# Performance work log

Measured on AMD Instinct MI355X. Metric: run time of the kernel, lower is better.

The kernel has to match this reference:

```python
import jax, jax.numpy as jnp
import numpy as np

N_NODES = 100000
N_EDGES = 1200000
N_GRAPHS = 1000
HID = 64
OUT = 4
ALPHA_FLAG = 0.03
NEG_SLOPE = 0.2


def _glorot(key, shape):
    fan_in, fan_out = shape[0], shape[-1]
    lim = (6.0 / (fan_in + fan_out)) ** 0.5
    return jax.random.uniform(key, shape, jnp.float32, -lim, lim)


def setup_inputs() -> dict:
    key = jax.random.key(0)
    ks = jax.random.split(key, 32)
    inp = {
        "x": jax.random.normal(ks[0], (N_NODES, 8), jnp.float32),
        "edge_index": jax.random.randint(ks[1], (2, N_EDGES), 0, N_NODES, jnp.int32),
        "batch": jnp.sort(jax.random.randint(ks[2], (N_NODES,), 0, N_GRAPHS, jnp.int32)),
        "climber": jax.random.normal(ks[3], (N_GRAPHS, 6), jnp.float32),
        # lin_in
        "W_in": _glorot(ks[4], (6, HID)), "b_in": jnp.zeros((HID,), jnp.float32),
        # climber_embed: LayerNorm(6) + Linear(6,64)
        "ln_g": jnp.ones((6,), jnp.float32), "ln_b": jnp.zeros((6,), jnp.float32),
        "W_c": _glorot(ks[5], (6, HID)), "b_c": jnp.zeros((HID,), jnp.float32),
        # film1 / film2: Linear(64,128)
        "Wf1": _glorot(ks[6], (HID, 2 * HID)), "bf1": jnp.zeros((2 * HID,), jnp.float32),
        "Wf2": _glorot(ks[7], (HID, 2 * HID)), "bf2": jnp.zeros((2 * HID,), jnp.float32),
        # GATConv 1 (heads=1): lin weight, att_src, att_dst, bias
        "Wg1": _glorot(ks[8], (HID, HID)), "as1": _glorot(ks[9], (HID, 1))[:, 0],
        "ad1": _glorot(ks[10], (HID, 1))[:, 0], "bg1": jnp.zeros((HID,), jnp.float32),
        # GATConv 2
        "Wg2": _glorot(ks[11], (HID, HID)), "as2": _glorot(ks[12], (HID, 1))[:, 0],
        "ad2": _glorot(ks[13], (HID, 1))[:, 0], "bg2": jnp.zeros((HID,), jnp.float32),
        # cls head
        "Wc1": _glorot(ks[14], (HID, HID)), "bc1": jnp.zeros((HID,), jnp.float32),
        "Wc2": _glorot(ks[15], (HID, OUT)), "bc2": jnp.zeros((OUT,), jnp.float32),
        # flag head
        "Wh1": _glorot(ks[16], (2, 8)), "bh1": jnp.zeros((8,), jnp.float32),
        "Wh2": _glorot(ks[17], (8, OUT)), "bh2": jnp.zeros((OUT,), jnp.float32),
    }
    return inp


def _gat(h, src, dst, W, a_src, a_dst, bias, n):
    # PyG GATConv, heads=1, concat=False, self-loops already appended.
    z = h @ W                                    # [N, H]
    e = jax.nn.leaky_relu((z @ a_src)[src] + (z @ a_dst)[dst], NEG_SLOPE)  # [E]
    m = jax.ops.segment_max(e, dst, num_segments=n)
    ex = jnp.exp(e - m[dst])
    s = jax.ops.segment_sum(ex, dst, num_segments=n)
    alpha = ex / (s[dst] + 1e-16)
    out = jax.ops.segment_sum(alpha[:, None] * z[src], dst, num_segments=n)
    return out + bias


def reference(x, edge_index, batch, climber, W_in, b_in, ln_g, ln_b, W_c, b_c,
              Wf1, bf1, Wf2, bf2, Wg1, as1, ad1, bg1, Wg2, as2, ad2, bg2,
              Wc1, bc1, Wc2, bc2, Wh1, bh1, Wh2, bh2):
    n = x.shape[0]
    # add self loops (PyG GATConv default)
    loop = jnp.arange(n, dtype=edge_index.dtype)
    src = jnp.concatenate([edge_index[0], loop])
    dst = jnp.concatenate([edge_index[1], loop])

    x_cont, flags = x[:, :6], x[:, 6:8]
    h = x_cont @ W_in + b_in

    # climber embed: LayerNorm + Linear + ReLU
    mu = jnp.mean(climber, -1, keepdims=True)
    var = jnp.var(climber, -1, keepdims=True)
    cn = (climber - mu) * jax.lax.rsqrt(var + 1e-5) * ln_g + ln_b
    c = jax.nn.relu(cn @ W_c + b_c)

    def film(h, Wf, bf):
        gb = c @ Wf + bf
        gamma, beta = jnp.split(gb, 2, axis=-1)
        return h * (1.0 + gamma[batch]) + beta[batch]

    h = film(h, Wf1, bf1)
    h = jax.nn.relu(_gat(h, src, dst, Wg1, as1, ad1, bg1, n))
    h = film(h, Wf2, bf2)
    h = jax.nn.relu(_gat(h, src, dst, Wg2, as2, ad2, bg2, n))

    # cls head (dropout inactive in eval)
    cls = jax.nn.relu(h @ Wc1 + bc1) @ Wc2 + bc2
    flag = jax.nn.relu(flags @ Wh1 + bh1) @ Wh2 + bh2
    return cls + ALPHA_FLAG * flag
```

## Files before the change

### kernel.cpp

```cpp
#include <hip/hip_runtime.h>
#include <math.h>

#define N_NODES 100000
#define N_EDGES 1200000
#define N_GRAPHS 1000
#define HID 64
#define NBUCK 256
#define NPB   391
#define BCAP  8192
#define EDGE_CHUNK 16384
#define S3_BLOCKS ((N_EDGES + EDGE_CHUNK - 1) / EDGE_CHUNK)
#define LOG2E 1.4426950408889634f
#define N_TILES (N_NODES / 16)
#define MFMA_BLOCKS 391

typedef _Float16 half_t;
typedef __attribute__((ext_vector_type(4))) _Float16 half4;
typedef __attribute__((ext_vector_type(8))) _Float16 half8;
typedef __attribute__((ext_vector_type(4))) float floatx4;

__global__ void k_climber_film(const float* __restrict__ climber,
                               const float* __restrict__ ln_g, const float* __restrict__ ln_b,
                               const float* __restrict__ W_c, const float* __restrict__ b_c,
                               const float* __restrict__ Wf1, const float* __restrict__ bf1,
                               const float* __restrict__ Wf2, const float* __restrict__ bf2,
                               float* __restrict__ gb1, float* __restrict__ gb2,
                               int* __restrict__ bucket_fill) {
    __shared__ float cl[64];
    int g = blockIdx.x;
    int j = threadIdx.x;
    if (g == 0) {
        bucket_fill[j] = 0;
        bucket_fill[j + 128] = 0;
    }
    if (j < 64) {
        float v[6];
        float mu = 0.f;
        #pragma unroll
        for (int k = 0; k < 6; k++) { v[k] = climber[g*6+k]; mu += v[k]; }
        mu *= (1.f/6.f);
        float var = 0.f;
        #pragma unroll
        for (int k = 0; k < 6; k++) { float d = v[k]-mu; var += d*d; }
        var *= (1.f/6.f);
        float rs = rsqrtf(var + 1e-5f);
        float acc = b_c[j];
        #pragma unroll
        for (int k = 0; k < 6; k++) {
            float cn = (v[k]-mu)*rs*ln_g[k] + ln_b[k];
            acc += cn * W_c[k*64+j];
        }
        cl[j] = fmaxf(acc, 0.f);
    }
    __syncthreads();
    float a1 = bf1[j], a2 = bf2[j];
    #pragma unroll 8
    for (int k = 0; k < 64; k++) {
        float ck = cl[k];
        a1 += ck * Wf1[k*128+j];
        a2 += ck * Wf2[k*128+j];
    }
    gb1[g*128+j] = a1;
    gb2[g*128+j] = a2;
}


__global__ void k_bin(const int* __restrict__ ei, int* __restrict__ bucket_fill,
                      int* __restrict__ staged) {
    __shared__ int hist[NBUCK];
    __shared__ int cursor[NBUCK];
    for (int t = threadIdx.x; t < NBUCK; t += blockDim.x) hist[t] = 0;
    __syncthreads();
    int e0 = blockIdx.x * EDGE_CHUNK;
    int e1 = min(e0 + EDGE_CHUNK, N_EDGES);
    for (int e = e0 + threadIdx.x; e < e1; e += blockDim.x)
        atomicAdd(&hist[ei[N_EDGES + e] / NPB], 1);
    __syncthreads();
    if (threadIdx.x < NBUCK) {
        int hv = hist[threadIdx.x];
        int start = threadIdx.x * BCAP;
        if (hv) start += atomicAdd(&bucket_fill[threadIdx.x], hv);
        cursor[threadIdx.x] = start;
    }
    __syncthreads();
    for (int e = e0 + threadIdx.x; e < e1; e += blockDim.x) {
        int src = ei[e], dst = ei[N_EDGES + e];
        int b = dst / NPB;
        int ldst = dst - b * NPB;
        int pos = atomicAdd(&cursor[b], 1);
        staged[pos] = (ldst << 17) | src;
    }
}

__global__ void k_bcsr(const int* __restrict__ staged, const int* __restrict__ bucket_fill,
                       int* __restrict__ rowptr, int* __restrict__ csr_src) {
    __shared__ int bb[NBUCK];
    __shared__ int ldeg[NPB];
    __shared__ int sc[512];
    __shared__ int cursor[NPB];
    int b = blockIdx.x;
    if (threadIdx.x < NBUCK) bb[threadIdx.x] = bucket_fill[threadIdx.x];
    __syncthreads();
    for (int off = 1; off < NBUCK; off <<= 1) {
        int u = 0;
        if (threadIdx.x < NBUCK && threadIdx.x >= off) u = bb[threadIdx.x - off];
        __syncthreads();
        if (threadIdx.x < NBUCK) bb[threadIdx.x] += u;
        __syncthreads();
    }
    int bbase = (b == 0) ? 0 : bb[b-1];
    int bcnt  = bb[b] - bbase;
    const int* st = staged + b * BCAP;
    int n0 = b * NPB;
    int n1 = min(n0 + NPB, N_NODES);
    int nn = n1 - n0;
    for (int t = threadIdx.x; t < NPB; t += blockDim.x) ldeg[t] = 0;
    __syncthreads();
    for (int k = threadIdx.x; k < bcnt; k += blockDim.x)
        atomicAdd(&ldeg[st[k] >> 17], 1);
    __syncthreads();
    if (threadIdx.x < 512) sc[threadIdx.x] = (threadIdx.x < nn) ? ldeg[threadIdx.x] : 0;
    __syncthreads();
    for (int off = 1; off < 512; off <<= 1) {
        int u = 0;
        if (threadIdx.x < 512 && threadIdx.x >= off) u = sc[threadIdx.x - off];
        __syncthreads();
        if (threadIdx.x < 512) sc[threadIdx.x] += u;
        __syncthreads();
    }
    if (threadIdx.x < nn) {
        int pre = sc[threadIdx.x] - ldeg[threadIdx.x];
        rowptr[n0 + threadIdx.x] = bbase + pre;
        cursor[threadIdx.x] = bbase + pre;
    }
    if (b == 0 && threadIdx.x == 0) rowptr[N_NODES] = bb[NBUCK-1];
    __syncthreads();
    for (int k = threadIdx.x; k < bcnt; k += blockDim.x) {
        int v = st[k];
        int pos = atomicAdd(&cursor[v >> 17], 1);
        csr_src[pos] = v & 0x1FFFF;
    }
}

__global__ __launch_bounds__(256) void k_mfma_z1(
        const float* __restrict__ x, const int* __restrict__ batch,
        const float* __restrict__ W_in, const float* __restrict__ b_in,
        const float* __restrict__ gb1, const float* __restrict__ W,
        const float* __restrict__ a_src, const float* __restrict__ a_dst,
        half_t* __restrict__ z, float* __restrict__ es, float* __restrict__ ed) {
    __shared__ float Wi[384];
    __shared__ float bi[64];
    __shared__ half_t zl[4][16*64];
    for (int idx = threadIdx.x; idx < 384; idx += 256) Wi[idx] = W_in[idx];
    if (threadIdx.x < 64) bi[threadIdx.x] = b_in[threadIdx.x];
    int wave = threadIdx.x >> 6;
    int l    = threadIdx.x & 63;
    int c    = l & 15;
    int g    = l >> 4;
    half8 Bf[2][4];
    #pragma unroll
    for (int ko = 0; ko < 2; ko++) {
        #pragma unroll
        for (int nt = 0; nt < 4; nt++) {
            half8 bvec;
            #pragma unroll
            for (int j = 0; j < 8; j++)
                bvec[j] = (half_t)W[(ko*32 + g*8 + j)*64 + c + 16*nt];
            Bf[ko][nt] = bvec;
        }
    }
    float as4[4], ad4[4];
    #pragma unroll
    for (int nt = 0; nt < 4; nt++) {
        as4[nt] = a_src[c + 16*nt] * LOG2E;
        ad4[nt] = a_dst[c + 16*nt] * LOG2E;
    }
    __syncthreads();
    int nWaves = gridDim.x * 4;
    int wid = blockIdx.x * 4 + wave;
    half_t* zw = zl[wave];
    for (int t = wid; t < N_TILES; t += nWaves) {
        int m0 = t * 16;
        int i = m0 + c;
        float xv[6];
        #pragma unroll
        for (int kk = 0; kk < 6; kk++) xv[kk] = x[i*8 + kk];
        int bg_ = batch[i];
        half8 A[2];
        #pragma unroll
        for (int s = 0; s < 2; s++) {
            int bk = s*32 + g*8;
            float acc[8];
            #pragma unroll
            for (int j = 0; j < 8; j++) acc[j] = bi[bk + j];
            #pragma unroll
            for (int kk = 0; kk < 6; kk++) {
                float xk = xv[kk];
                float4 w0 = *(const float4*)&Wi[kk*64 + bk];
                float4 w1 = *(const float4*)&Wi[kk*64 + bk + 4];
                acc[0] += xk*w0.x; acc[1] += xk*w0.y;
                acc[2] += xk*w0.z; acc[3] += xk*w0.w;
                acc[4] += xk*w1.x; acc[5] += xk*w1.y;
                acc[6] += xk*w1.z; acc[7] += xk*w1.w;
            }
            const float4* gbv = (const float4*)(gb1 + bg_*128);
            float4 ga0 = gbv[bk/4],      ga1 = gbv[bk/4 + 1];
            float4 be0 = gbv[16 + bk/4], be1 = gbv[16 + bk/4 + 1];
            half8 hv;
            hv[0] = (half_t)(acc[0]*(1.f+ga0.x) + be0.x);
            hv[1] = (half_t)(acc[1]*(1.f+ga0.y) + be0.y);
            hv[2] = (half_t)(acc[2]*(1.f+ga0.z) + be0.z);
            hv[3] = (half_t)(acc[3]*(1.f+ga0.w) + be0.w);
            hv[4] = (half_t)(acc[4]*(1.f+ga1.x) + be1.x);
            hv[5] = (half_t)(acc[5]*(1.f+ga1.y) + be1.y);
            hv[6] = (half_t)(acc[6]*(1.f+ga1.z) + be1.z);
            hv[7] = (half_t)(acc[7]*(1.f+ga1.w) + be1.w);
            A[s] = hv;
        }
        floatx4 D[4];
        #pragma unroll
        for (int nt = 0; nt < 4; nt++) {
            floatx4 acc = {0.f, 0.f, 0.f, 0.f};
            acc = __builtin_amdgcn_mfma_f32_16x16x32_f16(A[0], Bf[0][nt], acc, 0, 0, 0);
            acc = __builtin_amdgcn_mfma_f32_16x16x32_f16(A[1], Bf[1][nt], acc, 0, 0, 0);
            D[nt] = acc;
        }
        #pragma unroll
        for (int r = 0; r < 4; r++) {
            float ps = D[0][r]*as4[0] + D[1][r]*as4[1] + D[2][r]*as4[2] + D[3][r]*as4[3];
            float pd = D[0][r]*ad4[0] + D[1][r]*ad4[1] + D[2][r]*ad4[2] + D[3][r]*ad4[3];
            #pragma unroll
            for (int off = 1; off < 16; off <<= 1) {
                ps += __shfl_xor(ps, off, 16);
                pd += __shfl_xor(pd, off, 16);
            }
            if (c == 0) {
                es[m0 + g*4 + r] = ps;
                ed[m0 + g*4 + r] = pd;
            }
        }
        #pragma unroll
        for (int nt = 0; nt < 4; nt++) {
            #pragma unroll
            for (int r = 0; r < 4; r++)
                zw[(g*4 + r)*64 + c + 16*nt] = (half_t)D[nt][r];
        }
        __asm__ __volatile__("s_waitcnt lgkmcnt(0)" ::: "memory");
        const half8* zr = (const half8*)zw;
        half8 v0 = zr[l*2];
        half8 v1 = zr[l*2 + 1];
        half8* zo = (half8*)(z + (size_t)m0 * 64);
        zo[l*2]     = v0;
        zo[l*2 + 1] = v1;
        __asm__ __volatile__("s_waitcnt lgkmcnt(0)" ::: "memory");
    }
}

__global__ __launch_bounds__(256) void k_mfma_z(
        const half_t* __restrict__ h, const float* __restrict__ W,
        const float* __restrict__ a_src, const float* __restrict__ a_dst,
        half_t* __restrict__ z, float* __restrict__ es, float* __restrict__ ed) {
    __shared__ half_t zl[4][16*64];
    int wave = threadIdx.x >> 6;
    int l    = threadIdx.x & 63;
    int c    = l & 15;
    int g    = l >> 4;
    half8 Bf[2][4];
    #pragma unroll
    for (int ko = 0; ko < 2; ko++) {
        #pragma unroll
        for (int nt = 0; nt < 4; nt++) {
            half8 b;
            #pragma unroll
            for (int j = 0; j < 8; j++)
                b[j] = (half_t)W[(ko*32 + g*8 + j)*64 + c + 16*nt];
            Bf[ko][nt] = b;
        }
    }
    float as4[4], ad4[4];
    #pragma unroll
    for (int nt = 0; nt < 4; nt++) {
        as4[nt] = a_src[c + 16*nt] * LOG2E;
        ad4[nt] = a_dst[c + 16*nt] * LOG2E;
    }
    int nWaves = gridDim.x * 4;
    int wid = blockIdx.x * 4 + wave;
    half_t* zw = zl[wave];
    for (int t = wid; t < N_TILES; t += nWaves) {
        int m0 = t * 16;
        const half8* hrow = (const half8*)(h + (size_t)(m0 + c) * 64);
        half8 A0 = hrow[g];
        half8 A1 = hrow[g + 4];
        floatx4 D[4];
        #pragma unroll
        for (int nt = 0; nt < 4; nt++) {
            floatx4 acc = {0.f, 0.f, 0.f, 0.f};
            acc = __builtin_amdgcn_mfma_f32_16x16x32_f16(A0, Bf[0][nt], acc, 0, 0, 0);
            acc = __builtin_amdgcn_mfma_f32_16x16x32_f16(A1, Bf[1][nt], acc, 0, 0, 0);
            D[nt] = acc;
        }
        #pragma unroll
        for (int r = 0; r < 4; r++) {
            float ps = D[0][r]*as4[0] + D[1][r]*as4[1] + D[2][r]*as4[2] + D[3][r]*as4[3];
            float pd = D[0][r]*ad4[0] + D[1][r]*ad4[1] + D[2][r]*ad4[2] + D[3][r]*ad4[3];
            #pragma unroll
            for (int off = 1; off < 16; off <<= 1) {
                ps += __shfl_xor(ps, off, 16);
                pd += __shfl_xor(pd, off, 16);
            }
            if (c == 0) {
                es[m0 + g*4 + r] = ps;
                ed[m0 + g*4 + r] = pd;
            }
        }
        #pragma unroll
        for (int nt = 0; nt < 4; nt++) {
            #pragma unroll
            for (int r = 0; r < 4; r++)
                zw[(g*4 + r)*64 + c + 16*nt] = (half_t)D[nt][r];
        }
        __asm__ __volatile__("s_waitcnt lgkmcnt(0)" ::: "memory");
        const half8* zr = (const half8*)zw;
        half8 v0 = zr[l*2];
        half8 v1 = zr[l*2 + 1];
        half8* zo = (half8*)(z + (size_t)m0 * 64);
        zo[l*2]     = v0;
        zo[l*2 + 1] = v1;
        __asm__ __volatile__("s_waitcnt lgkmcnt(0)" ::: "memory");
    }
}

__device__ __forceinline__ float4 h4_to_f4(half4 h) {
    float4 f;
    f.x = (float)h.x; f.y = (float)h.y; f.z = (float)h.z; f.w = (float)h.w;
    return f;
}

__global__ void k_agg(const int* __restrict__ rowptr, const int* __restrict__ csr_src,
                      const float* __restrict__ es, const float* __restrict__ ed,
                      const half_t* __restrict__ z, const float* __restrict__ bg,
                      const int* __restrict__ batch, const float* __restrict__ gb,
                      int apply_film, half_t* __restrict__ hout) {
    int tid = blockIdx.x * blockDim.x + threadIdx.x;
    int i  = tid >> 4;
    int sl = threadIdx.x & 15;
    if (i >= N_NODES) return;
    int beg = rowptr[i], end = rowptr[i+1];
    int deg = end - beg;
    float edi = ed[i];

    float e_self = es[i] + edi;
    e_self = fmaxf(e_self, 0.2f * e_self);

    int svA = 0, svB = 0;
    float exA = 0.f, exB = 0.f;
    if (sl < deg) {
        svA = csr_src[beg + sl];
        float v = es[svA] + edi;
        exA = exp2f(fmaxf(v, 0.2f * v));
    }
    if (16 + sl < deg) {
        svB = csr_src[beg + 16 + sl];
        float v = es[svB] + edi;
        exB = exp2f(fmaxf(v, 0.2f * v));
    }
    float s = exA + exB;
    #pragma unroll
    for (int off = 1; off < 16; off <<= 1)
        s += __shfl_xor(s, off, 16);
    float ex = exp2f(e_self);
    s += ex;

    const half4* z4 = (const half4*)z;
    float4 zi = h4_to_f4(z4[i*16 + sl]);
    float4 acc = {ex*zi.x, ex*zi.y, ex*zi.z, ex*zi.w};

    int lim = (deg < 32) ? deg : 32;
    int k = 0;
    for (; k + 8 <= lim; k += 8) {
        int a[8]; float e[8];
        if (k < 16) {
            #pragma unroll
            for (int j = 0; j < 8; j++) {
                a[j] = __shfl(svA, k+j, 16);
                e[j] = __shfl(exA, k+j, 16);
            }
        } else {
            #pragma unroll
            for (int j = 0; j < 8; j++) {
                a[j] = __shfl(svB, k-16+j, 16);
                e[j] = __shfl(exB, k-16+j, 16);
            }
        }
        half4 q[8];
        #pragma unroll
        for (int j = 0; j < 8; j++) q[j] = z4[a[j]*16 + sl];
        #pragma unroll
        for (int j = 0; j < 8; j++) {
            float4 r = h4_to_f4(q[j]);
            acc.x += e[j]*r.x; acc.y += e[j]*r.y;
            acc.z += e[j]*r.z; acc.w += e[j]*r.w;
        }
    }
    for (; k + 4 <= lim; k += 4) {
        int a[4]; float e[4];
        if (k < 16) {
            #pragma unroll
            for (int j = 0; j < 4; j++) {
                a[j] = __shfl(svA, k+j, 16);
                e[j] = __shfl(exA, k+j, 16);
            }
        } else {
            #pragma unroll
            for (int j = 0; j < 4; j++) {
                a[j] = __shfl(svB, k-16+j, 16);
                e[j] = __shfl(exB, k-16+j, 16);
            }
        }
        half4 q[4];
        #pragma unroll
        for (int j = 0; j < 4; j++) q[j] = z4[a[j]*16 + sl];
        #pragma unroll
        for (int j = 0; j < 4; j++) {
            float4 r = h4_to_f4(q[j]);
            acc.x += e[j]*r.x; acc.y += e[j]*r.y;
            acc.z += e[j]*r.z; acc.w += e[j]*r.w;
        }
    }
    for (; k < lim; k++) {
        int a; float e2;
        if (k < 16) { a = __shfl(svA, k, 16);    e2 = __shfl(exA, k, 16); }
        else        { a = __shfl(svB, k-16, 16); e2 = __shfl(exB, k-16, 16); }
        float4 zr = h4_to_f4(z4[a*16 + sl]);
        acc.x += e2*zr.x; acc.y += e2*zr.y; acc.z += e2*zr.z; acc.w += e2*zr.w;
    }
    for (int kk = beg + 32; kk < end; kk++) {
        int sv = csr_src[kk];
        float v = es[sv] + edi;
        float e2 = exp2f(fmaxf(v, 0.2f * v));
        s += e2;
        float4 zr = h4_to_f4(z4[sv*16 + sl]);
        acc.x += e2*zr.x; acc.y += e2*zr.y; acc.z += e2*zr.z; acc.w += e2*zr.w;
    }
    float inv = 1.f / (s + 1e-16f);
    float4 bg4 = ((const float4*)bg)[sl];
    float4 o;
    o.x = fmaxf(acc.x*inv + bg4.x, 0.f);
    o.y = fmaxf(acc.y*inv + bg4.y, 0.f);
    o.z = fmaxf(acc.z*inv + bg4.z, 0.f);
    o.w = fmaxf(acc.w*inv + bg4.w, 0.f);
    if (apply_film) {
        int g = batch[i];
        const float4* gb4 = (const float4*)gb;
        float4 ga = gb4[g*32 + sl];
        float4 be = gb4[g*32 + 16 + sl];
        o.x = o.x*(1.f+ga.x) + be.x;
        o.y = o.y*(1.f+ga.y) + be.y;
        o.z = o.z*(1.f+ga.z) + be.z;
        o.w = o.w*(1.f+ga.w) + be.w;
    }
    half4 hv;
    hv.x = (half_t)o.x; hv.y = (half_t)o.y; hv.z = (half_t)o.z; hv.w = (half_t)o.w;
    ((half4*)hout)[i*16 + sl] = hv;
}

__global__ __launch_bounds__(256) void k_head_mfma(
        const half_t* __restrict__ h, const float* __restrict__ x,
        const float* __restrict__ Wc1, const float* __restrict__ bc1,
        const float* __restrict__ Wc2, const float* __restrict__ bc2,
        const float* __restrict__ Wh1, const float* __restrict__ bh1,
        const float* __restrict__ Wh2, const float* __restrict__ bh2,
        float* __restrict__ out) {
    int l    = threadIdx.x & 63;
    int c    = l & 15;
    int g    = l >> 4;
    half8 Bf[2][4];
    #pragma unroll
    for (int ko = 0; ko < 2; ko++) {
        #pragma unroll
        for (int nt = 0; nt < 4; nt++) {
            half8 b;
            #pragma unroll
            for (int j = 0; j < 8; j++)
                b[j] = (half_t)Wc1[(ko*32 + g*8 + j)*64 + c + 16*nt];
            Bf[ko][nt] = b;
        }
    }
    float bc1v[4];
    float4 w2[4];
    #pragma unroll
    for (int nt = 0; nt < 4; nt++) {
        bc1v[nt] = bc1[c + 16*nt];
        w2[nt] = ((const float4*)Wc2)[c + 16*nt];
    }
    int nWaves = gridDim.x * 4;
    int wid = blockIdx.x * 4 + (threadIdx.x >> 6);
    for (int t = wid; t < N_TILES; t += nWaves) {
        int m0 = t * 16;
        const half8* hrow = (const half8*)(h + (size_t)(m0 + c) * 64);
        half8 A0 = hrow[g];
        half8 A1 = hrow[g + 4];
        floatx4 D[4];
        #pragma unroll
        for (int nt = 0; nt < 4; nt++) {
            floatx4 acc = {0.f, 0.f, 0.f, 0.f};
            acc = __builtin_amdgcn_mfma_f32_16x16x32_f16(A0, Bf[0][nt], acc, 0, 0, 0);
            acc = __builtin_amdgcn_mfma_f32_16x16x32_f16(A1, Bf[1][nt], acc, 0, 0, 0);
            D[nt] = acc;
        }
        #pragma unroll
        for (int r = 0; r < 4; r++) {
            float4 p = {0.f, 0.f, 0.f, 0.f};
            #pragma unroll
            for (int nt = 0; nt < 4; nt++) {
                float tv = fmaxf(D[nt][r] + bc1v[nt], 0.f);
                p.x += tv * w2[nt].x;
                p.y += tv * w2[nt].y;
                p.z += tv * w2[nt].z;
                p.w += tv * w2[nt].w;
            }
            #pragma unroll
            for (int off = 1; off < 16; off <<= 1) {
                p.x += __shfl_xor(p.x, off, 16);
                p.y += __shfl_xor(p.y, off, 16);
                p.z += __shfl_xor(p.z, off, 16);
                p.w += __shfl_xor(p.w, off, 16);
            }
            if (c == 0) {
                int m = m0 + g*4 + r;
                float f0 = x[m*8+6], f1 = x[m*8+7];
                float t8[8];
                #pragma unroll
                for (int q = 0; q < 8; q++)
                    t8[q] = fmaxf(f0*Wh1[q] + f1*Wh1[8+q] + bh1[q], 0.f);
                float fl[4];
                #pragma unroll
                for (int q = 0; q < 4; q++) {
                    float a = bh2[q];
                    #pragma unroll
                    for (int rr = 0; rr < 8; rr++) a += t8[rr]*Wh2[rr*4+q];
                    fl[q] = a;
                }
                float4 ov;
                ov.x = p.x + bc2[0] + 0.03f*fl[0];
                ov.y = p.y + bc2[1] + 0.03f*fl[1];
                ov.z = p.z + bc2[2] + 0.03f*fl[2];
                ov.w = p.w + bc2[3] + 0.03f*fl[3];
                ((float4*)out)[m] = ov;
            }
        }
    }
}

extern "C" void kernel_launch(void* const* d_in, const int* in_sizes, int n_in,
                              void* d_out, int out_size, void* d_ws, size_t ws_size,
                              hipStream_t stream) {
    const float* x       = (const float*)d_in[0];
    const int*   ei      = (const int*)  d_in[1];
    const int*   batch   = (const int*)  d_in[2];
    const float* climber = (const float*)d_in[3];
    const float* W_in    = (const float*)d_in[4];
    const float* b_in    = (const float*)d_in[5];
    const float* ln_g    = (const float*)d_in[6];
    const float* ln_b    = (const float*)d_in[7];
    const float* W_c     = (const float*)d_in[8];
    const float* b_c     = (const float*)d_in[9];
    const float* Wf1     = (const float*)d_in[10];
    const float* bf1     = (const float*)d_in[11];
    const float* Wf2     = (const float*)d_in[12];
    const float* bf2     = (const float*)d_in[13];
    const float* Wg1     = (const float*)d_in[14];
    const float* as1     = (const float*)d_in[15];
    const float* ad1     = (const float*)d_in[16];
    const float* bg1     = (const float*)d_in[17];
    const float* Wg2     = (const float*)d_in[18];
    const float* as2     = (const float*)d_in[19];
    const float* ad2     = (const float*)d_in[20];
    const float* bg2     = (const float*)d_in[21];
    const float* Wc1     = (const float*)d_in[22];
    const float* bc1     = (const float*)d_in[23];
    const float* Wc2     = (const float*)d_in[24];
    const float* bc2     = (const float*)d_in[25];
    const float* Wh1     = (const float*)d_in[26];
    const float* bh1     = (const float*)d_in[27];
    const float* Wh2     = (const float*)d_in[28];
    const float* bh2     = (const float*)d_in[29];
    float* out = (float*)d_out;
    float* ws  = (float*)d_ws;

    float*  gb1         = ws;
    float*  gb2         = gb1 + 128000;
    half_t* hbuf        = (half_t*)(gb2 + 128000);
    half_t* zbuf        = hbuf + 6400000;
    float*  es          = (float*)(zbuf + 6400000);
    float*  ed          = es + N_NODES;
    int*    rowptr      = (int*)(ed + N_NODES);
    int*    csr_src     = rowptr + N_NODES + 1;
    int*    bucket_fill = csr_src + N_EDGES;
    int*    staged      = bucket_fill + NBUCK;

    k_climber_film<<<N_GRAPHS, 128, 0, stream>>>(climber, ln_g, ln_b, W_c, b_c,
                                                 Wf1, bf1, Wf2, bf2, gb1, gb2,
                                                 bucket_fill);

    k_bin <<<S3_BLOCKS, 1024, 0, stream>>>(ei, bucket_fill, staged);
    k_bcsr<<<NBUCK, 1024, 0, stream>>>(staged, bucket_fill, rowptr, csr_src);

    int nodeBlocks = (N_NODES*16 + 255)/256;
    k_mfma_z1<<<MFMA_BLOCKS, 256, 0, stream>>>(x, batch, W_in, b_in, gb1, Wg1,
                                               as1, ad1, zbuf, es, ed);
    k_agg<<<nodeBlocks, 256, 0, stream>>>(rowptr, csr_src, es, ed, zbuf, bg1,
                                          batch, gb2, 1, hbuf);
    k_mfma_z<<<MFMA_BLOCKS, 256, 0, stream>>>(hbuf, Wg2, as2, ad2, zbuf, es, ed);
    k_agg<<<nodeBlocks, 256, 0, stream>>>(rowptr, csr_src, es, ed, zbuf, bg2,
                                          batch, gb2, 0, hbuf);
    k_head_mfma<<<MFMA_BLOCKS, 256, 0, stream>>>(hbuf, x, Wc1, bc1, Wc2, bc2,
                                                 Wh1, bh1, Wh2, bh2, out);
}
```

Baseline: 259.3 us.

## Fuse GAT projection and head into aggregation kernels, merge CSR build with layer-1 projection

Folds the second-layer linear projection and attention-logit computation into the first aggregation kernel, and the classification head into the second aggregation kernel, so the intermediate h buffer is never written to or reread from global memory. The CSR finalisation and the layer-1 projection now run as one launch, with different block ranges doing each. Weights are pre-swizzled to fp16 MFMA layout by two extra blocks in the climber kernel. Edge chunk size for binning is also reduced. This removes three kernel launches and some global round-trips, at the cost of extra __syncthreads in the aggregation blocks and double-buffered z/es/ed.

```diff
diff --git a/kernel.cpp b/kernel.cpp
--- a/kernel.cpp
+++ b/kernel.cpp
@@ -8,11 +8,12 @@
 #define NBUCK 256
 #define NPB   391
 #define BCAP  8192
-#define EDGE_CHUNK 16384
+#define EDGE_CHUNK 4096
 #define S3_BLOCKS ((N_EDGES + EDGE_CHUNK - 1) / EDGE_CHUNK)
+#define Z1_BLOCKS 98
 #define LOG2E 1.4426950408889634f
 #define N_TILES (N_NODES / 16)
-#define MFMA_BLOCKS 391
+#define AGG_BLOCKS (N_NODES / 16)
 
 typedef _Float16 half_t;
 typedef __attribute__((ext_vector_type(4))) _Float16 half4;
@@ -24,11 +25,27 @@
                                const float* __restrict__ W_c, const float* __restrict__ b_c,
                                const float* __restrict__ Wf1, const float* __restrict__ bf1,
                                const float* __restrict__ Wf2, const float* __restrict__ bf2,
+                               const float* __restrict__ Wg2, const float* __restrict__ Wc1,
                                float* __restrict__ gb1, float* __restrict__ gb2,
+                               half_t* __restrict__ Wp1, half_t* __restrict__ Wp2,
                                int* __restrict__ bucket_fill) {
     __shared__ float cl[64];
     int g = blockIdx.x;
     int j = threadIdx.x;
+    if (g >= N_GRAPHS) {
+        const float* Wsrc = (g == N_GRAPHS) ? Wg2 : Wc1;
+        half_t*      Wdst = (g == N_GRAPHS) ? Wp1 : Wp2;
+        for (int idx = j; idx < 4096; idx += 128) {
+            int jj = idx & 7;
+            int ko = (idx >> 3) & 1;
+            int l  = (idx >> 4) & 63;
+            int w  = idx >> 10;
+            int c  = l & 15;
+            int gg = l >> 4;
+            Wdst[idx] = (half_t)Wsrc[(ko*32 + gg*8 + jj)*64 + c + 16*w];
+        }
+        return;
+    }
     if (g == 0) {
         bucket_fill[j] = 0;
         bucket_fill[j + 128] = 0;
@@ -64,9 +81,9 @@
     gb2[g*128+j] = a2;
 }
 
-
-__global__ void k_bin(const int* __restrict__ ei, int* __restrict__ bucket_fill,
-                      int* __restrict__ staged) {
+__global__ __launch_bounds__(1024) void k_bin(const int* __restrict__ ei,
+                                              int* __restrict__ bucket_fill,
+                                              int* __restrict__ staged) {
     __shared__ int hist[NBUCK];
     __shared__ int cursor[NBUCK];
     for (int t = threadIdx.x; t < NBUCK; t += blockDim.x) hist[t] = 0;
@@ -92,66 +109,67 @@
     }
 }
 
-__global__ void k_bcsr(const int* __restrict__ staged, const int* __restrict__ bucket_fill,
-                       int* __restrict__ rowptr, int* __restrict__ csr_src) {
-    __shared__ int bb[NBUCK];
-    __shared__ int ldeg[NPB];
-    __shared__ int sc[512];
-    __shared__ int cursor[NPB];
-    int b = blockIdx.x;
-    if (threadIdx.x < NBUCK) bb[threadIdx.x] = bucket_fill[threadIdx.x];
-    __syncthreads();
-    for (int off = 1; off < NBUCK; off <<= 1) {
-        int u = 0;
-        if (threadIdx.x < NBUCK && threadIdx.x >= off) u = bb[threadIdx.x - off];
-        __syncthreads();
-        if (threadIdx.x < NBUCK) bb[threadIdx.x] += u;
-        __syncthreads();
-    }
-    int bbase = (b == 0) ? 0 : bb[b-1];
-    int bcnt  = bb[b] - bbase;
-    const int* st = staged + b * BCAP;
-    int n0 = b * NPB;
-    int n1 = min(n0 + NPB, N_NODES);
-    int nn = n1 - n0;
-    for (int t = threadIdx.x; t < NPB; t += blockDim.x) ldeg[t] = 0;
-    __syncthreads();
-    for (int k = threadIdx.x; k < bcnt; k += blockDim.x)
-        atomicAdd(&ldeg[st[k] >> 17], 1);
-    __syncthreads();
-    if (threadIdx.x < 512) sc[threadIdx.x] = (threadIdx.x < nn) ? ldeg[threadIdx.x] : 0;
-    __syncthreads();
-    for (int off = 1; off < 512; off <<= 1) {
-        int u = 0;
-        if (threadIdx.x < 512 && threadIdx.x >= off) u = sc[threadIdx.x - off];
-        __syncthreads();
-        if (threadIdx.x < 512) sc[threadIdx.x] += u;
-        __syncthreads();
-    }
-    if (threadIdx.x < nn) {
-        int pre = sc[threadIdx.x] - ldeg[threadIdx.x];
-        rowptr[n0 + threadIdx.x] = bbase + pre;
-        cursor[threadIdx.x] = bbase + pre;
-    }
-    if (b == 0 && threadIdx.x == 0) rowptr[N_NODES] = bb[NBUCK-1];
-    __syncthreads();
-    for (int k = threadIdx.x; k < bcnt; k += blockDim.x) {
-        int v = st[k];
-        int pos = atomicAdd(&cursor[v >> 17], 1);
-        csr_src[pos] = v & 0x1FFFF;
-    }
-}
-
-__global__ __launch_bounds__(256) void k_mfma_z1(
+__global__ __launch_bounds__(1024) void k_mid(
+        const int* __restrict__ staged, const int* __restrict__ bucket_fill,
+        int* __restrict__ rowptr, int* __restrict__ csr_src,
         const float* __restrict__ x, const int* __restrict__ batch,
         const float* __restrict__ W_in, const float* __restrict__ b_in,
         const float* __restrict__ gb1, const float* __restrict__ W,
         const float* __restrict__ a_src, const float* __restrict__ a_dst,
         half_t* __restrict__ z, float* __restrict__ es, float* __restrict__ ed) {
+    if (blockIdx.x < NBUCK) {
+        __shared__ int bb[NBUCK];
+        __shared__ int ldeg[NPB];
+        __shared__ int sc[512];
+        __shared__ int cursor[NPB];
+        int b = blockIdx.x;
+        if (threadIdx.x < NBUCK) bb[threadIdx.x] = bucket_fill[threadIdx.x];
+        __syncthreads();
+        for (int off = 1; off < NBUCK; off <<= 1) {
+            int u = 0;
+            if (threadIdx.x < NBUCK && threadIdx.x >= off) u = bb[threadIdx.x - off];
+            __syncthreads();
+            if (threadIdx.x < NBUCK) bb[threadIdx.x] += u;
+            __syncthreads();
+        }
+        int bbase = (b == 0) ? 0 : bb[b-1];
+        int bcnt  = bb[b] - bbase;
+        const int* st = staged + b * BCAP;
+        int n0 = b * NPB;
+        int n1 = min(n0 + NPB, N_NODES);
+        int nn = n1 - n0;
+        for (int t = threadIdx.x; t < NPB; t += blockDim.x) ldeg[t] = 0;
+        __syncthreads();
+        for (int k = threadIdx.x; k < bcnt; k += blockDim.x)
+            atomicAdd(&ldeg[st[k] >> 17], 1);
+        __syncthreads();
+        if (threadIdx.x < 512) sc[threadIdx.x] = (threadIdx.x < nn) ? ldeg[threadIdx.x] : 0;
+        __syncthreads();
+        for (int off = 1; off < 512; off <<= 1) {
+            int u = 0;
+            if (threadIdx.x < 512 && threadIdx.x >= off) u = sc[threadIdx.x - off];
+            __syncthreads();
+            if (threadIdx.x < 512) sc[threadIdx.x] += u;
+            __syncthreads();
+        }
+        if (threadIdx.x < nn) {
+            int pre = sc[threadIdx.x] - ldeg[threadIdx.x];
+            rowptr[n0 + threadIdx.x] = bbase + pre;
+            cursor[threadIdx.x] = bbase + pre;
+        }
+        if (b == 0 && threadIdx.x == 0) rowptr[N_NODES] = bb[NBUCK-1];
+        __syncthreads();
+        for (int k = threadIdx.x; k < bcnt; k += blockDim.x) {
+            int v = st[k];
+            int pos = atomicAdd(&cursor[v >> 17], 1);
+            csr_src[pos] = v & 0x1FFFF;
+        }
+        return;
+    }
     __shared__ float Wi[384];
     __shared__ float bi[64];
-    __shared__ half_t zl[4][16*64];
-    for (int idx = threadIdx.x; idx < 384; idx += 256) Wi[idx] = W_in[idx];
+    __shared__ __align__(16) half_t zl[16][1024];
+    for (int idx = threadIdx.x; idx < 384; idx += 1024) Wi[idx] = W_in[idx];
     if (threadIdx.x < 64) bi[threadIdx.x] = b_in[threadIdx.x];
     int wave = threadIdx.x >> 6;
     int l    = threadIdx.x & 63;
@@ -176,8 +194,8 @@
         ad4[nt] = a_dst[c + 16*nt] * LOG2E;
     }
     __syncthreads();
-    int nWaves = gridDim.x * 4;
-    int wid = blockIdx.x * 4 + wave;
+    int nWaves = Z1_BLOCKS * 16;
+    int wid = (blockIdx.x - NBUCK) * 16 + wave;
     half_t* zw = zl[wave];
     for (int t = wid; t < N_TILES; t += nWaves) {
         int m0 = t * 16;
@@ -256,99 +274,39 @@
     }
 }
 
-__global__ __launch_bounds__(256) void k_mfma_z(
-        const half_t* __restrict__ h, const float* __restrict__ W,
-        const float* __restrict__ a_src, const float* __restrict__ a_dst,
-        half_t* __restrict__ z, float* __restrict__ es, float* __restrict__ ed) {
-    __shared__ half_t zl[4][16*64];
-    int wave = threadIdx.x >> 6;
-    int l    = threadIdx.x & 63;
-    int c    = l & 15;
-    int g    = l >> 4;
-    half8 Bf[2][4];
-    #pragma unroll
-    for (int ko = 0; ko < 2; ko++) {
-        #pragma unroll
-        for (int nt = 0; nt < 4; nt++) {
-            half8 b;
-            #pragma unroll
-            for (int j = 0; j < 8; j++)
-                b[j] = (half_t)W[(ko*32 + g*8 + j)*64 + c + 16*nt];
-            Bf[ko][nt] = b;
-        }
-    }
-    float as4[4], ad4[4];
-    #pragma unroll
-    for (int nt = 0; nt < 4; nt++) {
-        as4[nt] = a_src[c + 16*nt] * LOG2E;
-        ad4[nt] = a_dst[c + 16*nt] * LOG2E;
-    }
-    int nWaves = gridDim.x * 4;
-    int wid = blockIdx.x * 4 + wave;
-    half_t* zw = zl[wave];
-    for (int t = wid; t < N_TILES; t += nWaves) {
-        int m0 = t * 16;
-        const half8* hrow = (const half8*)(h + (size_t)(m0 + c) * 64);
-        half8 A0 = hrow[g];
-        half8 A1 = hrow[g + 4];
-        floatx4 D[4];
-        #pragma unroll
-        for (int nt = 0; nt < 4; nt++) {
-            floatx4 acc = {0.f, 0.f, 0.f, 0.f};
-            acc = __builtin_amdgcn_mfma_f32_16x16x32_f16(A0, Bf[0][nt], acc, 0, 0, 0);
-            acc = __builtin_amdgcn_mfma_f32_16x16x32_f16(A1, Bf[1][nt], acc, 0, 0, 0);
-            D[nt] = acc;
-        }
-        #pragma unroll
-        for (int r = 0; r < 4; r++) {
-            float ps = D[0][r]*as4[0] + D[1][r]*as4[1] + D[2][r]*as4[2] + D[3][r]*as4[3];
-            float pd = D[0][r]*ad4[0] + D[1][r]*ad4[1] + D[2][r]*ad4[2] + D[3][r]*ad4[3];
-            #pragma unroll
-            for (int off = 1; off < 16; off <<= 1) {
-                ps += __shfl_xor(ps, off, 16);
-                pd += __shfl_xor(pd, off, 16);
-            }
-            if (c == 0) {
-                es[m0 + g*4 + r] = ps;
-                ed[m0 + g*4 + r] = pd;
-            }
-        }
-        #pragma unroll
-        for (int nt = 0; nt < 4; nt++) {
-            #pragma unroll
-            for (int r = 0; r < 4; r++)
-                zw[(g*4 + r)*64 + c + 16*nt] = (half_t)D[nt][r];
-        }
-        __asm__ __volatile__("s_waitcnt lgkmcnt(0)" ::: "memory");
-        const half8* zr = (const half8*)zw;
-        half8 v0 = zr[l*2];
-        half8 v1 = zr[l*2 + 1];
-        half8* zo = (half8*)(z + (size_t)m0 * 64);
-        zo[l*2]     = v0;
-        zo[l*2 + 1] = v1;
-        __asm__ __volatile__("s_waitcnt lgkmcnt(0)" ::: "memory");
-    }
-}
-
 __device__ __forceinline__ float4 h4_to_f4(half4 h) {
     float4 f;
     f.x = (float)h.x; f.y = (float)h.y; f.z = (float)h.z; f.w = (float)h.w;
     return f;
 }
 
-__global__ void k_agg(const int* __restrict__ rowptr, const int* __restrict__ csr_src,
-                      const float* __restrict__ es, const float* __restrict__ ed,
-                      const half_t* __restrict__ z, const float* __restrict__ bg,
-                      const int* __restrict__ batch, const float* __restrict__ gb,
-                      int apply_film, half_t* __restrict__ hout) {
-    int tid = blockIdx.x * blockDim.x + threadIdx.x;
-    int i  = tid >> 4;
-    int sl = threadIdx.x & 15;
-    if (i >= N_NODES) return;
+template<int MODE>
+__global__ __launch_bounds__(256) void k_agg_f(
+        const int* __restrict__ rowptr, const int* __restrict__ csr_src,
+        const float* __restrict__ es, const float* __restrict__ ed,
+        const half_t* __restrict__ z, const float* __restrict__ bg,
+        const int* __restrict__ batch, const float* __restrict__ gb,
+        const half_t* __restrict__ Wp,
+        const float* __restrict__ av_s, const float* __restrict__ av_d,
+        half_t* __restrict__ zout, float* __restrict__ es_o, float* __restrict__ ed_o,
+        const float* __restrict__ x,
+        const float* __restrict__ bc1, const float* __restrict__ Wc2,
+        const float* __restrict__ bc2,
+        const float* __restrict__ Wh1, const float* __restrict__ bh1,
+        const float* __restrict__ Wh2, const float* __restrict__ bh2,
+        float* __restrict__ out) {
+    __shared__ __align__(16) half_t h_l[1024];
+    __shared__ __align__(16) half_t zl16[1024];
+    __shared__ float red[4][16][4];
+    int tidb = threadIdx.x;
+    int il = tidb >> 4;
+    int sl = tidb & 15;
+    int m0 = blockIdx.x * 16;
+    int i = m0 + il;
+
     int beg = rowptr[i], end = rowptr[i+1];
     int deg = end - beg;
     float edi = ed[i];
-
     float e_self = es[i] + edi;
     e_self = fmaxf(e_self, 0.2f * e_self);
 
@@ -449,11 +407,11 @@
     o.y = fmaxf(acc.y*inv + bg4.y, 0.f);
     o.z = fmaxf(acc.z*inv + bg4.z, 0.f);
     o.w = fmaxf(acc.w*inv + bg4.w, 0.f);
-    if (apply_film) {
-        int g = batch[i];
+    if (MODE == 1) {
+        int gidx = batch[i];
         const float4* gb4 = (const float4*)gb;
-        float4 ga = gb4[g*32 + sl];
-        float4 be = gb4[g*32 + 16 + sl];
+        float4 ga = gb4[gidx*32 + sl];
+        float4 be = gb4[gidx*32 + 16 + sl];
         o.x = o.x*(1.f+ga.x) + be.x;
         o.y = o.y*(1.f+ga.y) + be.y;
         o.z = o.z*(1.f+ga.z) + be.z;
@@ -461,93 +419,97 @@
     }
     half4 hv;
     hv.x = (half_t)o.x; hv.y = (half_t)o.y; hv.z = (half_t)o.z; hv.w = (half_t)o.w;
-    ((half4*)hout)[i*16 + sl] = hv;
-}
-
-__global__ __launch_bounds__(256) void k_head_mfma(
-        const half_t* __restrict__ h, const float* __restrict__ x,
-        const float* __restrict__ Wc1, const float* __restrict__ bc1,
-        const float* __restrict__ Wc2, const float* __restrict__ bc2,
-        const float* __restrict__ Wh1, const float* __restrict__ bh1,
-        const float* __restrict__ Wh2, const float* __restrict__ bh2,
-        float* __restrict__ out) {
-    int l    = threadIdx.x & 63;
+    *(half4*)((char*)h_l + il*128 + ((sl*8) ^ ((il & 7) << 4))) = hv;
+
+    int l    = tidb & 63;
+    int wave = tidb >> 6;
     int c    = l & 15;
     int g    = l >> 4;
-    half8 Bf[2][4];
-    #pragma unroll
-    for (int ko = 0; ko < 2; ko++) {
-        #pragma unroll
-        for (int nt = 0; nt < 4; nt++) {
-            half8 b;
-            #pragma unroll
-            for (int j = 0; j < 8; j++)
-                b[j] = (half_t)Wc1[(ko*32 + g*8 + j)*64 + c + 16*nt];
-            Bf[ko][nt] = b;
-        }
-    }
-    float bc1v[4];
-    float4 w2[4];
-    #pragma unroll
-    for (int nt = 0; nt < 4; nt++) {
-        bc1v[nt] = bc1[c + 16*nt];
-        w2[nt] = ((const float4*)Wc2)[c + 16*nt];
-    }
-    int nWaves = gridDim.x * 4;
-    int wid = blockIdx.x * 4 + (threadIdx.x >> 6);
-    for (int t = wid; t < N_TILES; t += nWaves) {
-        int m0 = t * 16;
-        const half8* hrow = (const half8*)(h + (size_t)(m0 + c) * 64);
-        half8 A0 = hrow[g];
-        half8 A1 = hrow[g + 4];
-        floatx4 D[4];
-        #pragma unroll
-        for (int nt = 0; nt < 4; nt++) {
-            floatx4 acc = {0.f, 0.f, 0.f, 0.f};
-            acc = __builtin_amdgcn_mfma_f32_16x16x32_f16(A0, Bf[0][nt], acc, 0, 0, 0);
-            acc = __builtin_amdgcn_mfma_f32_16x16x32_f16(A1, Bf[1][nt], acc, 0, 0, 0);
-            D[nt] = acc;
-        }
+    const half8* wp = (const half8*)(Wp + ((size_t)tidb << 4));
+    half8 Bf0 = wp[0];
+    half8 Bf1 = wp[1];
+    float as_w = 0.f, ad_w = 0.f, bc1w = 0.f;
+    float4 w2w = {0.f, 0.f, 0.f, 0.f};
+    if (MODE == 1) {
+        as_w = av_s[c + 16*wave] * LOG2E;
+        ad_w = av_d[c + 16*wave] * LOG2E;
+    } else {
+        bc1w = bc1[c + 16*wave];
+        w2w  = ((const float4*)Wc2)[c + 16*wave];
+    }
+    __syncthreads();
+    half8 A0 = *(const half8*)((const char*)h_l + c*128 + ((g*16)      ^ ((c & 7) << 4)));
+    half8 A1 = *(const half8*)((const char*)h_l + c*128 + ((64 + g*16) ^ ((c & 7) << 4)));
+    floatx4 D = {0.f, 0.f, 0.f, 0.f};
+    D = __builtin_amdgcn_mfma_f32_16x16x32_f16(A0, Bf0, D, 0, 0, 0);
+    D = __builtin_amdgcn_mfma_f32_16x16x32_f16(A1, Bf1, D, 0, 0, 0);
+    if (MODE == 1) {
         #pragma unroll
         for (int r = 0; r < 4; r++) {
-            float4 p = {0.f, 0.f, 0.f, 0.f};
-            #pragma unroll
-            for (int nt = 0; nt < 4; nt++) {
-                float tv = fmaxf(D[nt][r] + bc1v[nt], 0.f);
-                p.x += tv * w2[nt].x;
-                p.y += tv * w2[nt].y;
-                p.z += tv * w2[nt].z;
-                p.w += tv * w2[nt].w;
-            }
+            float ps = D[r]*as_w, pd = D[r]*ad_w;
             #pragma unroll
             for (int off = 1; off < 16; off <<= 1) {
-                p.x += __shfl_xor(p.x, off, 16);
-                p.y += __shfl_xor(p.y, off, 16);
-                p.z += __shfl_xor(p.z, off, 16);
-                p.w += __shfl_xor(p.w, off, 16);
+                ps += __shfl_xor(ps, off, 16);
+                pd += __shfl_xor(pd, off, 16);
             }
             if (c == 0) {
-                int m = m0 + g*4 + r;
-                float f0 = x[m*8+6], f1 = x[m*8+7];
-                float t8[8];
+                red[wave][g*4 + r][0] = ps;
+                red[wave][g*4 + r][1] = pd;
+            }
+            zl16[(g*4 + r)*64 + c + 16*wave] = (half_t)D[r];
+        }
+        __syncthreads();
+        if (tidb < 16) {
+            es_o[m0 + tidb] = red[0][tidb][0] + red[1][tidb][0] + red[2][tidb][0] + red[3][tidb][0];
+            ed_o[m0 + tidb] = red[0][tidb][1] + red[1][tidb][1] + red[2][tidb][1] + red[3][tidb][1];
+        }
+        if (tidb < 128)
+            ((half8*)(zout + (size_t)m0 * 64))[tidb] = ((const half8*)zl16)[tidb];
+    } else {
+        #pragma unroll
+        for (int r = 0; r < 4; r++) {
+            float tv = fmaxf(D[r] + bc1w, 0.f);
+            float px = tv*w2w.x, py = tv*w2w.y, pz = tv*w2w.z, pw = tv*w2w.w;
+            #pragma unroll
+            for (int off = 1; off < 16; off <<= 1) {
+                px += __shfl_xor(px, off, 16);
+                py += __shfl_xor(py, off, 16);
+                pz += __shfl_xor(pz, off, 16);
+                pw += __shfl_xor(pw, off, 16);
+            }
+            if (c == 0) {
+                red[wave][g*4 + r][0] = px;
+                red[wave][g*4 + r][1] = py;
+                red[wave][g*4 + r][2] = pz;
+                red[wave][g*4 + r][3] = pw;
+            }
+        }
+        __syncthreads();
+        if (tidb < 16) {
+            int m = m0 + tidb;
+            float p0 = red[0][tidb][0] + red[1][tidb][0] + red[2][tidb][0] + red[3][tidb][0] + bc2[0];
+            float p1 = red[0][tidb][1] + red[1][tidb][1] + red[2][tidb][1] + red[3][tidb][1] + bc2[1];
+            float p2 = red[0][tidb][2] + red[1][tidb][2] + red[2][tidb][2] + red[3][tidb][2] + bc2[2];
+            float p3 = red[0][tidb][3] + red[1][tidb][3] + red[2][tidb][3] + red[3][tidb][3] + bc2[3];
+            float f0 = x[m*8+6], f1 = x[m*8+7];
+            float t8[8];
+            #pragma unroll
+            for (int q = 0; q < 8; q++)
+                t8[q] = fmaxf(f0*Wh1[q] + f1*Wh1[8+q] + bh1[q], 0.f);
+            float fl[4];
+            #pragma unroll
+            for (int q = 0; q < 4; q++) {
+                float a = bh2[q];
                 #pragma unroll
-                for (int q = 0; q < 8; q++)
-                    t8[q] = fmaxf(f0*Wh1[q] + f1*Wh1[8+q] + bh1[q], 0.f);
-                float fl[4];
-                #pragma unroll
-                for (int q = 0; q < 4; q++) {
-                    float a = bh2[q];
-                    #pragma unroll
-                    for (int rr = 0; rr < 8; rr++) a += t8[rr]*Wh2[rr*4+q];
-                    fl[q] = a;
-                }
-                float4 ov;
-                ov.x = p.x + bc2[0] + 0.03f*fl[0];
-                ov.y = p.y + bc2[1] + 0.03f*fl[1];
-                ov.z = p.z + bc2[2] + 0.03f*fl[2];
-                ov.w = p.w + bc2[3] + 0.03f*fl[3];
-                ((float4*)out)[m] = ov;
-            }
+                for (int rr = 0; rr < 8; rr++) a += t8[rr]*Wh2[rr*4+q];
+                fl[q] = a;
+            }
+            float4 ov;
+            ov.x = p0 + 0.03f*fl[0];
+            ov.y = p1 + 0.03f*fl[1];
+            ov.z = p2 + 0.03f*fl[2];
+            ov.w = p3 + 0.03f*fl[3];
+            ((float4*)out)[m] = ov;
         }
     }
 }
@@ -590,30 +552,39 @@
 
     float*  gb1         = ws;
     float*  gb2         = gb1 + 128000;
-    half_t* hbuf        = (half_t*)(gb2 + 128000);
-    half_t* zbuf        = hbuf + 6400000;
-    float*  es          = (float*)(zbuf + 6400000);
-    float*  ed          = es + N_NODES;
-    int*    rowptr      = (int*)(ed + N_NODES);
+    half_t* Wp1         = (half_t*)(gb2 + 128000);
+    half_t* Wp2         = Wp1 + 4096;
+    half_t* zA          = Wp2 + 4096;
+    half_t* zB          = zA + 6400000;
+    float*  es1         = (float*)(zB + 6400000);
+    float*  ed1         = es1 + N_NODES;
+    float*  es2         = ed1 + N_NODES;
+    float*  ed2         = es2 + N_NODES;
+    int*    rowptr      = (int*)(ed2 + N_NODES);
     int*    csr_src     = rowptr + N_NODES + 1;
     int*    bucket_fill = csr_src + N_EDGES;
     int*    staged      = bucket_fill + NBUCK;
 
-    k_climber_film<<<N_GRAPHS, 128, 0, stream>>>(climber, ln_g, ln_b, W_c, b_c,
-                                                 Wf1, bf1, Wf2, bf2, gb1, gb2,
-                                                 bucket_fill);
-
-    k_bin <<<S3_BLOCKS, 1024, 0, stream>>>(ei, bucket_fill, staged);
-    k_bcsr<<<NBUCK, 1024, 0, stream>>>(staged, bucket_fill, rowptr, csr_src);
-
-    int nodeBlocks = (N_NODES*16 + 255)/256;
-    k_mfma_z1<<<MFMA_BLOCKS, 256, 0, stream>>>(x, batch, W_in, b_in, gb1, Wg1,
-                                               as1, ad1, zbuf, es, ed);
-    k_agg<<<nodeBlocks, 256, 0, stream>>>(rowptr, csr_src, es, ed, zbuf, bg1,
-                                          batch, gb2, 1, hbuf);
-    k_mfma_z<<<MFMA_BLOCKS, 256, 0, stream>>>(hbuf, Wg2, as2, ad2, zbuf, es, ed);
-    k_agg<<<nodeBlocks, 256, 0, stream>>>(rowptr, csr_src, es, ed, zbuf, bg2,
-                                          batch, gb2, 0, hbuf);
-    k_head_mfma<<<MFMA_BLOCKS, 256, 0, stream>>>(hbuf, x, Wc1, bc1, Wc2, bc2,
-                                                 Wh1, bh1, Wh2, bh2, out);
+    k_climber_film<<<N_GRAPHS + 2, 128, 0, stream>>>(climber, ln_g, ln_b, W_c, b_c,
+                                                     Wf1, bf1, Wf2, bf2, Wg2, Wc1,
+                                                     gb1, gb2, Wp1, Wp2, bucket_fill);
+
+    k_bin<<<S3_BLOCKS, 1024, 0, stream>>>(ei, bucket_fill, staged);
+
+    k_mid<<<NBUCK + Z1_BLOCKS, 1024, 0, stream>>>(staged, bucket_fill, rowptr, csr_src,
+                                                  x, batch, W_in, b_in, gb1, Wg1,
+                                                  as1, ad1, zA, es1, ed1);
+
+    k_agg_f<1><<<AGG_BLOCKS, 256, 0, stream>>>(rowptr, csr_src, es1, ed1, zA, bg1,
+                                               batch, gb2, Wp1, as2, ad2,
+                                               zB, es2, ed2,
+                                               nullptr, nullptr, nullptr, nullptr,
+                                               nullptr, nullptr, nullptr, nullptr,
+                                               nullptr);
+
+    k_agg_f<2><<<AGG_BLOCKS, 256, 0, stream>>>(rowptr, csr_src, es2, ed2, zB, bg2,
+                                               batch, nullptr, Wp2, nullptr, nullptr,
+                                               nullptr, nullptr, nullptr,
+                                               x, bc1, Wc2, bc2, Wh1, bh1, Wh2, bh2,
+                                               out);
 }
```

After: 251.4 us. 3.0% less time.
